# Kernel tuning notes

Measured on AMD Instinct MI355X. Metric: run time of the kernel, lower is better.

The kernel has to match this reference:

```python
import jax, jax.numpy as jnp
import numpy as np

N = 50000          # nodes
E_RAND = 800000    # random edges (avg degree 16); self-loops appended per PyG GATConv default
IN = 128
HID = 32
HEADS = 4
OUT = 32
NEG_SLOPE = 0.2    # PyG GATConv default LeakyReLU slope


def setup_inputs() -> dict:
    key = jax.random.key(0)
    ks = jax.random.split(key, 8)
    x = jax.random.normal(ks[0], (N, IN), dtype=jnp.float32)
    src = jax.random.randint(ks[1], (E_RAND,), 0, N)
    dst = jax.random.randint(ks[2], (E_RAND,), 0, N)
    loops = jnp.arange(N)
    src = jnp.concatenate([src, loops])  # [E] with self-loops
    dst = jnp.concatenate([dst, loops])
    inp = {"x": x, "src": src, "dst": dst}
    layer_dims = [(IN, HID), (HID * HEADS, HID), (HID * HEADS, OUT)]
    for l, (din, c) in enumerate(layer_dims):
        k1, k2, k3 = jax.random.split(ks[3 + l], 3)
        s = 1.0 / np.sqrt(din)
        inp[f"W{l}"] = jax.random.uniform(k1, (HEADS * c, din), jnp.float32, -s, s)
        inp[f"asrc{l}"] = jax.random.uniform(k2, (HEADS, c), jnp.float32, -s, s)
        inp[f"adst{l}"] = jax.random.uniform(k3, (HEADS, c), jnp.float32, -s, s)
        inp[f"b{l}"] = jnp.zeros((HEADS * c,), jnp.float32)
    return inp


def _gat_conv(x, src, dst, W, a_src, a_dst, b):
    H, C = a_src.shape
    h = (x @ W.T).reshape(-1, H, C)                     # [N, H, C]
    al_s = jnp.einsum('nhc,hc->nh', h, a_src)           # node-level src score
    al_d = jnp.einsum('nhc,hc->nh', h, a_dst)           # node-level dst score
    e = jax.nn.leaky_relu(al_s[src] + al_d[dst], NEG_SLOPE)  # [E, H]
    # segment softmax over edges sharing the same destination node
    e_max = jax.ops.segment_max(e, dst, num_segments=N)
    e = jnp.exp(e - e_max[dst])
    denom = jax.ops.segment_sum(e, dst, num_segments=N)
    alpha = e / (denom[dst] + 1e-16)                    # [E, H]
    out = jax.ops.segment_sum(alpha[:, :, None] * h[src], dst, num_segments=N)  # [N, H, C]
    return out.reshape(-1, H * C) + b


def reference(x, src, dst, W0, asrc0, adst0, b0, W1, asrc1, adst1, b1, W2, asrc2, adst2, b2):
    params = [(W0, asrc0, adst0, b0), (W1, asrc1, adst1, b1), (W2, asrc2, adst2, b2)]
    h = x
    for i, (W, a_s, a_d, b) in enumerate(params):
        h = _gat_conv(h, src, dst, W, a_s, a_d, b)
        if i != len(params) - 1:
            h = jax.nn.elu(h)  # dropout p=0.5 is identity in eval mode
    return h
```

## Files before the change

### kernel.cpp

```cpp
#include <hip/hip_runtime.h>
#include <stdint.h>

typedef unsigned short ushort_t;
typedef unsigned int uint32;

typedef __attribute__((ext_vector_type(8))) short short8;
typedef __attribute__((ext_vector_type(4))) float floatx4;

#define NEG_SLOPE 0.2f

__device__ __forceinline__ ushort_t f2bf(float f) {
    union { float f; uint32 u; } v; v.f = f;
    uint32 u = v.u;
    uint32 r = (u + 0x7fffu + ((u >> 16) & 1u)) >> 16;
    return (ushort_t)r;
}
__device__ __forceinline__ float2 bf2x(uint32 u) {
    union { uint32 u; float f; } a, b;
    a.u = u << 16; b.u = u & 0xffff0000u;
    float2 r; r.x = a.f; r.y = b.f; return r;
}

__global__ void k_sniff(const uint32* __restrict__ x, int* __restrict__ flag) {
    __shared__ int sh[256];
    int t = threadIdx.x;
    int c = 0;
    for (int i = t; i < 1024; i += 256) {
        uint32 h = x[i] & 0xFFFFu;
        uint32 e = (h >> 7) & 0xFFu;
        if (h == 0u || (e >= 100u && e <= 140u)) c++;
    }
    sh[t] = c; __syncthreads();
    for (int off = 128; off >= 1; off >>= 1) {
        if (t < off) sh[t] += sh[t + off];
        __syncthreads();
    }
    if (t == 0) flag[0] = (sh[0] >= 512) ? 1 : 0;
}

__device__ __forceinline__ void gemm_body(int bid, int tid,
                                          const void* __restrict__ actv,
                                          const ushort_t* __restrict__ W,
                                          ushort_t* __restrict__ hb,
                                          float* __restrict__ als,
                                          float* __restrict__ ald,
                                          const ushort_t* __restrict__ asrcp,
                                          const ushort_t* __restrict__ adstp,
                                          int N, int layer0,
                                          const int* __restrict__ flag) {
    int wid = tid >> 6, lane = tid & 63;
    int n0 = (bid * 4 + wid) * 16;
    int mrow = lane & 15, quad = lane >> 4;
    int n = n0 + mrow;
    bool isf32 = (layer0 && !flag[0]);
    short8 a[4];
    if (n < N) {
        if (isf32) {
            const float* ar = (const float*)actv + (size_t)n * 128 + quad * 8;
            #pragma unroll
            for (int kt = 0; kt < 4; kt++) {
                float4 fa = *(const float4*)(ar + kt * 32);
                float4 fb = *(const float4*)(ar + kt * 32 + 4);
                short8 v;
                v[0] = (short)f2bf(fa.x); v[1] = (short)f2bf(fa.y);
                v[2] = (short)f2bf(fa.z); v[3] = (short)f2bf(fa.w);
                v[4] = (short)f2bf(fb.x); v[5] = (short)f2bf(fb.y);
                v[6] = (short)f2bf(fb.z); v[7] = (short)f2bf(fb.w);
                a[kt] = v;
            }
        } else {
            const ushort_t* ar = (const ushort_t*)actv + (size_t)n * 128 + quad * 8;
            #pragma unroll
            for (int kt = 0; kt < 4; kt++) a[kt] = *(const short8*)(ar + kt * 32);
        }
    } else {
        #pragma unroll
        for (int kt = 0; kt < 4; kt++) { short8 z = {0,0,0,0,0,0,0,0}; a[kt] = z; }
    }
    float ps[4], pd[4];
    #pragma unroll
    for (int t = 0; t < 8; t++) {
        if ((t & 1) == 0) {
            #pragma unroll
            for (int r = 0; r < 4; r++) { ps[r] = 0.f; pd[r] = 0.f; }
        }
        const ushort_t* wr = W + (size_t)(t * 16 + mrow) * 128 + quad * 8;
        floatx4 acc = {0.f, 0.f, 0.f, 0.f};
        #pragma unroll
        for (int kt = 0; kt < 4; kt++) {
            short8 b = *(const short8*)(wr + kt * 32);
            acc = __builtin_amdgcn_mfma_f32_16x16x32_bf16(a[kt], b, acc, 0, 0, 0);
        }
        int col = t * 16 + mrow;
        union { uint32 u; float f; } cs, cd;
        cs.u = ((uint32)asrcp[col]) << 16;
        cd.u = ((uint32)adstp[col]) << 16;
        #pragma unroll
        for (int r = 0; r < 4; r++) {
            int rn = n0 + quad * 4 + r;
            if (rn < N) hb[(size_t)rn * 128 + col] = f2bf(acc[r]);
            ps[r] += acc[r] * cs.f;
            pd[r] += acc[r] * cd.f;
        }
        if (t & 1) {
            #pragma unroll
            for (int off = 1; off <= 8; off <<= 1) {
                #pragma unroll
                for (int r = 0; r < 4; r++) {
                    ps[r] += __shfl_xor(ps[r], off);
                    pd[r] += __shfl_xor(pd[r], off);
                }
            }
            int h = t >> 1;
            if (mrow < 8) {
                int r = mrow & 3;
                float vs = r == 0 ? ps[0] : r == 1 ? ps[1] : r == 2 ? ps[2] : ps[3];
                float vd = r == 0 ? pd[0] : r == 1 ? pd[1] : r == 2 ? pd[2] : pd[3];
                int rn = n0 + quad * 4 + r;
                if (rn < N) {
                    float* dp = (mrow < 4) ? als : ald;
                    dp[(size_t)rn * 4 + h] = (mrow < 4) ? vs : vd;
                }
            }
        }
    }
}

__global__ __launch_bounds__(256) void k_gemm(const void* __restrict__ actv,
                                              const ushort_t* __restrict__ W,
                                              ushort_t* __restrict__ hb,
                                              float* __restrict__ als,
                                              float* __restrict__ ald,
                                              const ushort_t* __restrict__ asrcp,
                                              const ushort_t* __restrict__ adstp,
                                              int N, const int* __restrict__ flag) {
    gemm_body(blockIdx.x, threadIdx.x, actv, W, hb, als, ald, asrcp, adstp, N, 0, flag);
}

__global__ void k_f1(const void* W0, const void* W1, const void* W2,
                     const void* s0, const void* s1, const void* s2,
                     const void* a0, const void* a1, const void* a2,
                     const void* b0, const void* b1, const void* b2,
                     ushort_t* __restrict__ pblk, const int* __restrict__ flag,
                     const int* __restrict__ dst, int* __restrict__ cnt,
                     int* __restrict__ rank, int E) {
    if (blockIdx.x < 197) {
        int i = blockIdx.x * 256 + threadIdx.x;
        if (i >= 50304) return;
        const void* src; int off;
        if (i < 49152) {
            int seg = i / 16384; off = i % 16384;
            src = seg == 0 ? W0 : seg == 1 ? W1 : W2;
        } else if (i < 49536) {
            int j = i - 49152; int seg = j / 128; off = j % 128;
            src = seg == 0 ? s0 : seg == 1 ? s1 : s2;
        } else if (i < 49920) {
            int j = i - 49536; int seg = j / 128; off = j % 128;
            src = seg == 0 ? a0 : seg == 1 ? a1 : a2;
        } else {
            int j = i - 49920; int seg = j / 128; off = j % 128;
            src = seg == 0 ? b0 : seg == 1 ? b1 : b2;
        }
        if (flag[0]) pblk[i] = ((const ushort_t*)src)[off];
        else         pblk[i] = f2bf(((const float*)src)[off]);
    } else {
        int e0 = ((blockIdx.x - 197) * 256 + threadIdx.x) * 4;
        if (e0 + 3 < E) {
            int4 d4 = *(const int4*)(dst + e0);
            int r0 = atomicAdd(&cnt[d4.x], 1);
            int r1 = atomicAdd(&cnt[d4.y], 1);
            int r2 = atomicAdd(&cnt[d4.z], 1);
            int r3 = atomicAdd(&cnt[d4.w], 1);
            int4 r4 = {r0, r1, r2, r3};
            *(int4*)(rank + e0) = r4;
        } else {
            for (int e = e0; e < E; e++) rank[e] = atomicAdd(&cnt[dst[e]], 1);
        }
    }
}

__global__ __launch_bounds__(256) void k_f2(const int* __restrict__ cnt, int* __restrict__ ro,
                                            int* __restrict__ bsum, int n, int nb,
                                            const void* __restrict__ actv,
                                            const ushort_t* __restrict__ W,
                                            ushort_t* __restrict__ hb,
                                            float* __restrict__ als, float* __restrict__ ald,
                                            const ushort_t* __restrict__ asrcp,
                                            const ushort_t* __restrict__ adstp,
                                            int N, const int* __restrict__ flag) {
    if ((int)blockIdx.x < nb) {
        __shared__ int sd[256];
        int t = threadIdx.x;
        int base = blockIdx.x * 1024 + t * 4;
        int v0 = (base + 0 < n) ? cnt[base + 0] : 0;
        int v1 = (base + 1 < n) ? cnt[base + 1] : 0;
        int v2 = (base + 2 < n) ? cnt[base + 2] : 0;
        int v3 = (base + 3 < n) ? cnt[base + 3] : 0;
        int s = v0 + v1 + v2 + v3;
        sd[t] = s; __syncthreads();
        for (int off = 1; off < 256; off <<= 1) {
            int x = 0;
            if (t >= off) x = sd[t - off];
            __syncthreads();
            sd[t] += x;
            __syncthreads();
        }
        int run = sd[t] - s;
        run += v0; if (base + 0 < n) ro[base + 1] = run;
        run += v1; if (base + 1 < n) ro[base + 2] = run;
        run += v2; if (base + 2 < n) ro[base + 3] = run;
        run += v3; if (base + 3 < n) ro[base + 4] = run;
        if (t == 255) bsum[blockIdx.x] = sd[255];
    } else {
        gemm_body(blockIdx.x - nb, threadIdx.x, actv, W, hb, als, ald, asrcp, adstp, N, 1, flag);
    }
}

__global__ void k_scan_bc(int* __restrict__ ro, const int* __restrict__ bsum,
                          int n, int nb) {
    __shared__ int pre[256];
    int t = threadIdx.x;
    if (t == 0) {
        int acc = 0;
        for (int b = 0; b < nb; b++) { pre[b] = acc; acc += bsum[b]; }
    }
    __syncthreads();
    int i = blockIdx.x * 256 + t;
    if (i == 0) ro[0] = 0;
    if (i < n) ro[i + 1] += pre[i >> 10];
}

__global__ void k_scatter(const int* __restrict__ src, const int* __restrict__ dst,
                          const int* __restrict__ ro, const int* __restrict__ rank,
                          ushort_t* __restrict__ ssrc, int E) {
    int e0 = (blockIdx.x * 256 + threadIdx.x) * 4;
    if (e0 + 3 < E) {
        int4 d4 = *(const int4*)(dst + e0);
        int4 s4 = *(const int4*)(src + e0);
        int4 r4 = *(const int4*)(rank + e0);
        ssrc[ro[d4.x] + r4.x] = (ushort_t)s4.x;
        ssrc[ro[d4.y] + r4.y] = (ushort_t)s4.y;
        ssrc[ro[d4.z] + r4.z] = (ushort_t)s4.z;
        ssrc[ro[d4.w] + r4.w] = (ushort_t)s4.w;
    } else {
        for (int e = e0; e < E; e++) ssrc[ro[dst[e]] + rank[e]] = (ushort_t)src[e];
    }
}

__global__ __launch_bounds__(256) void k_agg(const int* __restrict__ ro,
                                             const ushort_t* __restrict__ ssrc,
                                             const ushort_t* __restrict__ hb,
                                             const float* __restrict__ als,
                                             const float* __restrict__ ald_,
                                             const ushort_t* __restrict__ bias,
                                             void* __restrict__ outp, int N, int apply_elu,
                                             int is_final, const int* __restrict__ flag) {
    int wid = threadIdx.x >> 6;
    int lane = threadIdx.x & 63;
    int n = blockIdx.x * 4 + wid;

    __shared__ __align__(16) float wsm[4][256];
    __shared__ int osm[4][64];

    if (n >= N) return;

    int r0 = ro[n], r1 = ro[n + 1];
    floatx4 ad = *(const floatx4*)(ald_ + (size_t)n * 4);
    const char* alsb = (const char*)als;
    float* wsm_ = &wsm[wid][0];
    int* osm_ = &osm[wid][0];

    int grp = lane >> 4;
    int sub = lane & 15;
    int hd = sub >> 2;

    float acc[8];
    #pragma unroll
    for (int k = 0; k < 8; k++) acc[k] = 0.f;
    float d0 = 0.f, d1 = 0.f, d2 = 0.f, d3 = 0.f;

    for (int base = r0; base < r1; base += 64) {
        int i = base + lane;
        if (i < r1) {
            int s = ssrc[i];
            floatx4 as = *(const floatx4*)(alsb + (s << 4));
            float t0 = as.x + ad.x; float w0 = __expf(fmaxf(t0, NEG_SLOPE * t0)); d0 += w0;
            float t1 = as.y + ad.y; float w1 = __expf(fmaxf(t1, NEG_SLOPE * t1)); d1 += w1;
            float t2 = as.z + ad.z; float w2 = __expf(fmaxf(t2, NEG_SLOPE * t2)); d2 += w2;
            float t3 = as.w + ad.w; float w3 = __expf(fmaxf(t3, NEG_SLOPE * t3)); d3 += w3;
            osm_[lane] = s << 8;
            floatx4 w4 = {w0, w1, w2, w3};
            *(floatx4*)(wsm_ + lane * 4) = w4;
        }
        __builtin_amdgcn_wave_barrier();
        int cend = min(64, r1 - base);
        int jfull = cend & ~3;
        #pragma unroll 4
        for (int j = 0; j < jfull; j += 4) {
            int je = j + grp;
            float wj = wsm_[je * 4 + hd];
            const char* rp = (const char*)hb + (uint32)osm_[je] + (sub << 4);
            short8 hv = *(const short8*)rp;
            #pragma unroll
            for (int k = 0; k < 8; k++) {
                union { uint32 u; float f; } c;
                c.u = ((uint32)(ushort_t)hv[k]) << 16;
                acc[k] += wj * c.f;
            }
        }
        if (jfull + grp < cend) {
            int je = jfull + grp;
            float wj = wsm_[je * 4 + hd];
            const char* rp = (const char*)hb + (uint32)osm_[je] + (sub << 4);
            short8 hv = *(const short8*)rp;
            #pragma unroll
            for (int k = 0; k < 8; k++) {
                union { uint32 u; float f; } c;
                c.u = ((uint32)(ushort_t)hv[k]) << 16;
                acc[k] += wj * c.f;
            }
        }
        __builtin_amdgcn_wave_barrier();
    }
    #pragma unroll
    for (int k = 0; k < 8; k++) {
        acc[k] += __shfl_xor(acc[k], 16);
        acc[k] += __shfl_xor(acc[k], 32);
    }
    #pragma unroll
    for (int off = 32; off >= 1; off >>= 1) {
        d0 += __shfl_xor(d0, off); d1 += __shfl_xor(d1, off);
        d2 += __shfl_xor(d2, off); d3 += __shfl_xor(d3, off);
    }
    if (grp == 0) {
        float den = (hd == 0 ? d0 : hd == 1 ? d1 : hd == 2 ? d2 : d3) + 1e-16f;
        float inv = 1.0f / den;
        int c0 = sub << 3;
        short8 bv8 = *(const short8*)(bias + c0);
        float o[8];
        #pragma unroll
        for (int k = 0; k < 8; k++) {
            union { uint32 u; float f; } b;
            b.u = ((uint32)(ushort_t)bv8[k]) << 16;
            o[k] = acc[k] * inv + b.f;
            if (apply_elu) o[k] = o[k] > 0.f ? o[k] : __expf(o[k]) - 1.f;
        }
        if (is_final && !flag[0]) {
            float* op = (float*)outp + (size_t)n * 128 + c0;
            float4 lo = {o[0], o[1], o[2], o[3]};
            float4 hi = {o[4], o[5], o[6], o[7]};
            *(float4*)op = lo;
            *(float4*)(op + 4) = hi;
        } else {
            short8 pk;
            #pragma unroll
            for (int k = 0; k < 8; k++) pk[k] = (short)f2bf(o[k]);
            *(short8*)((ushort_t*)outp + (size_t)n * 128 + c0) = pk;
        }
    }
}

extern "C" void kernel_launch(void* const* d_in, const int* in_sizes, int n_in,
                              void* d_out, int out_size, void* d_ws, size_t ws_size,
                              hipStream_t stream) {
    const void* x = d_in[0];
    const int* src = (const int*)d_in[1];
    const int* dst = (const int*)d_in[2];
    const int N = in_sizes[0] / 128;
    const int E = in_sizes[1];

    char* p = (char*)d_ws;
    auto alloc = [&](size_t bytes) { char* r = p; p += (bytes + 255) & ~(size_t)255; return r; };
    int*      flag  = (int*)alloc(256);
    int*      bsum  = (int*)alloc(256 * 4);
    int*      ro    = (int*)alloc((size_t)(N + 1) * 4);
    ushort_t* ssrc  = (ushort_t*)alloc((size_t)E * 2);
    ushort_t* hb    = (ushort_t*)alloc((size_t)N * 128 * 2);
    float*    als   = (float*)alloc((size_t)N * 4 * 4);
    float*    ald   = (float*)alloc((size_t)N * 4 * 4);
    ushort_t* xact  = (ushort_t*)alloc((size_t)N * 128 * 2);
    ushort_t* pblk  = (ushort_t*)alloc((size_t)50304 * 2);

    int* cnt  = (int*)ssrc;
    int* rank = (int*)xact;

    int g256e4 = (E + 1023) / 1024;
    int g256n = (N + 255) / 256;
    int nb = (N + 1023) / 1024;
    int gg = (N + 63) / 64;
    int gagg = (N + 3) / 4;

    k_sniff<<<1, 256, 0, stream>>>((const uint32*)x, flag);
    hipMemsetAsync(cnt, 0, (size_t)N * 4, stream);
    k_f1<<<197 + g256e4, 256, 0, stream>>>(
        d_in[3], d_in[7], d_in[11],
        d_in[4], d_in[8], d_in[12],
        d_in[5], d_in[9], d_in[13],
        d_in[6], d_in[10], d_in[14],
        pblk, flag, dst, cnt, rank, E);
    k_f2<<<nb + gg, 256, 0, stream>>>(cnt, ro, bsum, N, nb,
        x, pblk, hb, als, ald, pblk + 49152, pblk + 49536, N, flag);
    k_scan_bc<<<g256n, 256, 0, stream>>>(ro, bsum, N, nb);
    k_scatter<<<g256e4, 256, 0, stream>>>(src, dst, ro, rank, ssrc, E);

    for (int l = 0; l < 3; l++) {
        const ushort_t* As = pblk + 49152 + l * 128;
        const ushort_t* Ad = pblk + 49536 + l * 128;
        const ushort_t* Bc = pblk + 49920 + l * 128;
        void* outp = (l == 2) ? d_out : (void*)xact;
        if (l > 0) {
            const ushort_t* Wc = pblk + (size_t)l * 16384;
            k_gemm<<<gg, 256, 0, stream>>>(xact, Wc, hb, als, ald, As, Ad, N, flag);
        }
        k_agg<<<gagg, 256, 0, stream>>>(ro, ssrc, hb, als, ald, Bc, outp, N, l < 2 ? 1 : 0,
                                        l == 2 ? 1 : 0, flag);
    }
}
```

Before: 345.4 us.

## Compute attention weights per edge inline in aggregation, drop LDS staging

The aggregation kernel no longer stages per-edge softmax weights and source offsets through shared memory in chunks of 64. Each 16-lane group now processes its own edges directly: it loads the source index, computes the exp-leaky-relu weight for its head, and accumulates the bf16 row using packed float2 FMAs. This removes the LDS writes and reads, the wave barriers and the separate denominator shuffle over four heads. In exchange, the exp and the alpha_src load are repeated once per lane group for each edge, and the source-index loads are less coalesced.

```diff
diff --git a/kernel.cpp b/kernel.cpp
--- a/kernel.cpp
+++ b/kernel.cpp
@@ -6,6 +6,8 @@
 
 typedef __attribute__((ext_vector_type(8))) short short8;
 typedef __attribute__((ext_vector_type(4))) float floatx4;
+typedef __attribute__((ext_vector_type(2))) float float2v;
+typedef __attribute__((ext_vector_type(4))) uint32 uint4v;
 
 #define NEG_SLOPE 0.2f
 
@@ -258,92 +260,82 @@
     int wid = threadIdx.x >> 6;
     int lane = threadIdx.x & 63;
     int n = blockIdx.x * 4 + wid;
-
-    __shared__ __align__(16) float wsm[4][256];
-    __shared__ int osm[4][64];
-
     if (n >= N) return;
 
     int r0 = ro[n], r1 = ro[n + 1];
-    floatx4 ad = *(const floatx4*)(ald_ + (size_t)n * 4);
-    const char* alsb = (const char*)als;
-    float* wsm_ = &wsm[wid][0];
-    int* osm_ = &osm[wid][0];
-
     int grp = lane >> 4;
     int sub = lane & 15;
     int hd = sub >> 2;
 
-    float acc[8];
+    float adh = ald_[(size_t)n * 4 + hd];
+    const char* alsb = (const char*)als;
+    const char* hbb = (const char*)hb;
+    int hoff = hd << 2;
+    int coff = sub << 4;
+
+    float2v acc2[4];
     #pragma unroll
-    for (int k = 0; k < 8; k++) acc[k] = 0.f;
-    float d0 = 0.f, d1 = 0.f, d2 = 0.f, d3 = 0.f;
-
-    for (int base = r0; base < r1; base += 64) {
-        int i = base + lane;
-        if (i < r1) {
-            int s = ssrc[i];
-            floatx4 as = *(const floatx4*)(alsb + (s << 4));
-            float t0 = as.x + ad.x; float w0 = __expf(fmaxf(t0, NEG_SLOPE * t0)); d0 += w0;
-            float t1 = as.y + ad.y; float w1 = __expf(fmaxf(t1, NEG_SLOPE * t1)); d1 += w1;
-            float t2 = as.z + ad.z; float w2 = __expf(fmaxf(t2, NEG_SLOPE * t2)); d2 += w2;
-            float t3 = as.w + ad.w; float w3 = __expf(fmaxf(t3, NEG_SLOPE * t3)); d3 += w3;
-            osm_[lane] = s << 8;
-            floatx4 w4 = {w0, w1, w2, w3};
-            *(floatx4*)(wsm_ + lane * 4) = w4;
-        }
-        __builtin_amdgcn_wave_barrier();
-        int cend = min(64, r1 - base);
-        int jfull = cend & ~3;
-        #pragma unroll 4
-        for (int j = 0; j < jfull; j += 4) {
-            int je = j + grp;
-            float wj = wsm_[je * 4 + hd];
-            const char* rp = (const char*)hb + (uint32)osm_[je] + (sub << 4);
-            short8 hv = *(const short8*)rp;
-            #pragma unroll
-            for (int k = 0; k < 8; k++) {
-                union { uint32 u; float f; } c;
-                c.u = ((uint32)(ushort_t)hv[k]) << 16;
-                acc[k] += wj * c.f;
-            }
-        }
-        if (jfull + grp < cend) {
-            int je = jfull + grp;
-            float wj = wsm_[je * 4 + hd];
-            const char* rp = (const char*)hb + (uint32)osm_[je] + (sub << 4);
-            short8 hv = *(const short8*)rp;
-            #pragma unroll
-            for (int k = 0; k < 8; k++) {
-                union { uint32 u; float f; } c;
-                c.u = ((uint32)(ushort_t)hv[k]) << 16;
-                acc[k] += wj * c.f;
-            }
-        }
-        __builtin_amdgcn_wave_barrier();
+    for (int k = 0; k < 4; k++) { float2v z = {0.f, 0.f}; acc2[k] = z; }
+    float d = 0.f;
+
+    int i = r0 + grp;
+    int nfull = (r1 - r0) >> 2;
+    #pragma unroll 2
+    for (int t = 0; t < nfull; t++, i += 4) {
+        int s = ssrc[i];
+        float asv = *(const float*)(alsb + (s << 4) + hoff);
+        float tv = asv + adh;
+        float w = __expf(fmaxf(tv, NEG_SLOPE * tv));
+        d += w;
+        uint4v hv = *(const uint4v*)(hbb + (s << 8) + coff);
+        #pragma unroll
+        for (int k = 0; k < 4; k++) {
+            float2 p = bf2x(hv[k]);
+            float2v pv = {p.x, p.y};
+            acc2[k] += w * pv;
+        }
+    }
+    if (i < r1) {
+        int s = ssrc[i];
+        float asv = *(const float*)(alsb + (s << 4) + hoff);
+        float tv = asv + adh;
+        float w = __expf(fmaxf(tv, NEG_SLOPE * tv));
+        d += w;
+        uint4v hv = *(const uint4v*)(hbb + (s << 8) + coff);
+        #pragma unroll
+        for (int k = 0; k < 4; k++) {
+            float2 p = bf2x(hv[k]);
+            float2v pv = {p.x, p.y};
+            acc2[k] += w * pv;
+        }
     }
     #pragma unroll
-    for (int k = 0; k < 8; k++) {
-        acc[k] += __shfl_xor(acc[k], 16);
-        acc[k] += __shfl_xor(acc[k], 32);
-    }
-    #pragma unroll
-    for (int off = 32; off >= 1; off >>= 1) {
-        d0 += __shfl_xor(d0, off); d1 += __shfl_xor(d1, off);
-        d2 += __shfl_xor(d2, off); d3 += __shfl_xor(d3, off);
-    }
+    for (int k = 0; k < 4; k++) {
+        acc2[k].x += __shfl_xor(acc2[k].x, 16);
+        acc2[k].y += __shfl_xor(acc2[k].y, 16);
+        acc2[k].x += __shfl_xor(acc2[k].x, 32);
+        acc2[k].y += __shfl_xor(acc2[k].y, 32);
+    }
+    d += __shfl_xor(d, 16);
+    d += __shfl_xor(d, 32);
+
     if (grp == 0) {
-        float den = (hd == 0 ? d0 : hd == 1 ? d1 : hd == 2 ? d2 : d3) + 1e-16f;
-        float inv = 1.0f / den;
+        float inv = 1.0f / (d + 1e-16f);
         int c0 = sub << 3;
         short8 bv8 = *(const short8*)(bias + c0);
         float o[8];
         #pragma unroll
-        for (int k = 0; k < 8; k++) {
-            union { uint32 u; float f; } b;
-            b.u = ((uint32)(ushort_t)bv8[k]) << 16;
-            o[k] = acc[k] * inv + b.f;
-            if (apply_elu) o[k] = o[k] > 0.f ? o[k] : __expf(o[k]) - 1.f;
+        for (int k = 0; k < 4; k++) {
+            union { uint32 u; float f; } blo, bhi;
+            blo.u = ((uint32)(ushort_t)bv8[2 * k]) << 16;
+            bhi.u = ((uint32)(ushort_t)bv8[2 * k + 1]) << 16;
+            o[2 * k]     = acc2[k].x * inv + blo.f;
+            o[2 * k + 1] = acc2[k].y * inv + bhi.f;
+        }
+        if (apply_elu) {
+            #pragma unroll
+            for (int k = 0; k < 8; k++)
+                o[k] = o[k] > 0.f ? o[k] : __expf(o[k]) - 1.f;
         }
         if (is_final && !flag[0]) {
             float* op = (float*)outp + (size_t)n * 128 + c0;
```

Result: no change. 339.2 us (-1.8%).
